# Kernel tuning notes

Hardware: AMD Instinct MI355X
Metric: run time of the kernel (lower is better)

## Reference

```python
import jax, jax.numpy as jnp
import numpy as np

B, H, S, D = 2, 16, 2048, 64
EMBED_SIZE = 64
NEG_INF = -1e9


def setup_inputs() -> dict:
    key = jax.random.key(0)
    kq, kk, kv, kb = jax.random.split(key, 4)
    Q = jax.random.normal(kq, (B, H, S, D), dtype=jnp.float32)
    K = jax.random.normal(kk, (B, H, S, D), dtype=jnp.float32)
    V = jax.random.normal(kv, (B, H, S, D), dtype=jnp.float32)
    attn_bias = jax.random.normal(kb, (B, H, S, S), dtype=jnp.float32)
    # causal mask: True means masked (matches torch masked_fill semantics)
    causal = ~jnp.tril(jnp.ones((S, S), dtype=bool))
    attn_mask = jnp.broadcast_to(causal, (B, H, S, S))
    return {"Q": Q, "K": K, "V": V, "attn_mask": attn_mask, "attn_bias": attn_bias}


def reference(Q, K, V, attn_mask, attn_bias):
    scale = 1.0 / np.sqrt(EMBED_SIZE).astype(np.float32)
    scores = jnp.einsum("bhqd,bhkd->bhqk", Q, K) * scale  # [B,H,S,S]
    scores = scores + attn_bias
    scores = jnp.where(attn_mask, NEG_INF, scores)
    attn = jax.nn.softmax(scores, axis=-1)
    context = jnp.einsum("bhqk,bhkd->bhqd", attn, V)
    return (context, attn)
```

## Files before the change

kernel.cpp:

```cpp
#include <hip/hip_runtime.h>


typedef __attribute__((ext_vector_type(4))) float  f32x4;
typedef __attribute__((ext_vector_type(8))) short  short8;
typedef __attribute__((ext_vector_type(4))) short  short4v;

#define S_DIM 2048
#define D_DIM 64
#define QB    16

__device__ __forceinline__ unsigned short f2bf(float f) {
  unsigned u = __builtin_bit_cast(unsigned, f);
  u = (u + 0x7FFFu + ((u >> 16) & 1u)) >> 16;
  return (unsigned short)u;
}
__device__ __forceinline__ float bf2f(unsigned short s) {
  unsigned u = ((unsigned)s) << 16;
  return __builtin_bit_cast(float, u);
}

__launch_bounds__(256, 2)
__global__ void sdpa_kernel(const float* __restrict__ Qg,
                            const float* __restrict__ Kg,
                            const float* __restrict__ Vg,
                            const float* __restrict__ Bg,
                            float* __restrict__ ctx_out,
                            float* __restrict__ attn_out) {
  __shared__ unsigned short plds[QB * S_DIM];
  __shared__ unsigned short vt[D_DIM * 72];
  __shared__ float rowsum[QB];

  const int tid  = threadIdx.x;
  const int lane = tid & 63;
  const int wave = tid >> 6;
  const int l15  = lane & 15;
  const int l4   = lane >> 4;

  const int qtile = 127 - (int)blockIdx.x;
  const int bh    = blockIdx.y;
  const int qbase = qtile * QB;

  if (tid < QB) rowsum[tid] = 0.0f;
  __syncthreads();

  const float* qrow = Qg + ((size_t)bh * S_DIM + (size_t)(qbase + l15)) * D_DIM;
  short8 qfrag[2];
#pragma unroll
  for (int t = 0; t < 2; ++t) {
    const f32x4* p = (const f32x4*)(qrow + t * 32 + l4 * 8);
    f32x4 a = p[0], b = p[1];
    short8 f;
#pragma unroll
    for (int j = 0; j < 4; ++j) {
      f[j]     = (short)f2bf(a[j] * 0.125f);
      f[j + 4] = (short)f2bf(b[j] * 0.125f);
    }
    qfrag[t] = f;
  }

  const int nkt = ((qbase + QB - 1) >> 6) + 1;
  const float* Kbh = Kg + (size_t)bh * S_DIM * D_DIM;
  const float* Bbh = Bg + (size_t)bh * S_DIM * S_DIM;

  float rsv[4] = {0.f, 0.f, 0.f, 0.f};

  for (int kt = 0; kt < nkt; ++kt) {
    const int kg = kt * 64 + wave * 16 + l15;
    const float* krow = Kbh + (size_t)kg * D_DIM;
    short8 kfrag[2];
#pragma unroll
    for (int t = 0; t < 2; ++t) {
      const f32x4* p = (const f32x4*)(krow + t * 32 + l4 * 8);
      f32x4 a = p[0], b = p[1];
      short8 f;
#pragma unroll
      for (int j = 0; j < 4; ++j) {
        f[j]     = (short)f2bf(a[j]);
        f[j + 4] = (short)f2bf(b[j]);
      }
      kfrag[t] = f;
    }
    float bv[4];
#pragma unroll
    for (int r = 0; r < 4; ++r) {
      const int q = qbase + l4 * 4 + r;
      bv[r] = Bbh[(size_t)q * S_DIM + kg];
    }
    f32x4 acc = {0.f, 0.f, 0.f, 0.f};
    acc = __builtin_amdgcn_mfma_f32_16x16x32_bf16(qfrag[0], kfrag[0], acc, 0, 0, 0);
    acc = __builtin_amdgcn_mfma_f32_16x16x32_bf16(qfrag[1], kfrag[1], acc, 0, 0, 0);
#pragma unroll
    for (int r = 0; r < 4; ++r) {
      const int qi = l4 * 4 + r;
      const int q  = qbase + qi;
      const float pval = (kg <= q) ? __expf(acc[r] + bv[r]) : 0.0f;
      rsv[r] += pval;
      const int idx = (qi * S_DIM + kg) ^ ((qi & 7) << 3);
      plds[idx] = f2bf(pval);
    }
  }

#pragma unroll
  for (int r = 0; r < 4; ++r) {
    float v = rsv[r];
    v += __shfl_xor(v, 1);
    v += __shfl_xor(v, 2);
    v += __shfl_xor(v, 4);
    v += __shfl_xor(v, 8);
    if (l15 == 0) atomicAdd(&rowsum[l4 * 4 + r], v);
  }
  __syncthreads();

  float* abase = attn_out + ((size_t)bh * S_DIM + (size_t)qbase) * S_DIM;
  for (int qi = 0; qi < QB; ++qi) {
    const int qg = qbase + qi;
    const float inv = __builtin_amdgcn_rcpf(rowsum[qi]);
    float* arow = abase + (size_t)qi * S_DIM;
#pragma unroll
    for (int half = 0; half < 2; ++half) {
      const int kc = (half * 256 + tid) * 4;
      f32x4 o;
      if (kc > qg) {
        o = (f32x4){0.f, 0.f, 0.f, 0.f};
      } else {
        const int idx = (qi * S_DIM + kc) ^ ((qi & 7) << 3);
        short4v sv = *(const short4v*)&plds[idx];
#pragma unroll
        for (int j = 0; j < 4; ++j)
          o[j] = (kc + j <= qg) ? bf2f((unsigned short)sv[j]) * inv : 0.f;
      }
      *(f32x4*)(arow + kc) = o;
    }
  }

  f32x4 cacc = {0.f, 0.f, 0.f, 0.f};
  const float* Vbh = Vg + (size_t)bh * S_DIM * D_DIM;
  const int dbase = wave * 16;
  for (int kt = 0; kt < nkt; ++kt) {
    const float* vrow = Vbh + ((size_t)(kt * 64 + lane)) * D_DIM + dbase;
    f32x4 v0 = ((const f32x4*)vrow)[0];
    f32x4 v1 = ((const f32x4*)vrow)[1];
    f32x4 v2 = ((const f32x4*)vrow)[2];
    f32x4 v3 = ((const f32x4*)vrow)[3];
#pragma unroll
    for (int j = 0; j < 4; ++j) {
      vt[(dbase + j)      * 72 + lane] = f2bf(v0[j]);
      vt[(dbase + 4 + j)  * 72 + lane] = f2bf(v1[j]);
      vt[(dbase + 8 + j)  * 72 + lane] = f2bf(v2[j]);
      vt[(dbase + 12 + j) * 72 + lane] = f2bf(v3[j]);
    }
#pragma unroll
    for (int t = 0; t < 2; ++t) {
      const int kk   = kt * 64 + t * 32 + l4 * 8;
      const int aidx = (l15 * S_DIM + kk) ^ ((l15 & 7) << 3);
      short8 af = *(const short8*)&plds[aidx];
      short8 bf = *(const short8*)&vt[(dbase + l15) * 72 + t * 32 + l4 * 8];
      cacc = __builtin_amdgcn_mfma_f32_16x16x32_bf16(af, bf, cacc, 0, 0, 0);
    }
  }

  float* cbase = ctx_out + ((size_t)bh * S_DIM + (size_t)qbase) * D_DIM + dbase + l15;
#pragma unroll
  for (int r = 0; r < 4; ++r) {
    const int qi = l4 * 4 + r;
    const float inv = __builtin_amdgcn_rcpf(rowsum[qi]);
    cbase[(size_t)qi * D_DIM] = cacc[r] * inv;
  }
}

extern "C" void kernel_launch(void* const* d_in, const int* in_sizes, int n_in,
                              void* d_out, int out_size, void* d_ws, size_t ws_size,
                              hipStream_t stream) {
  (void)in_sizes; (void)n_in; (void)out_size; (void)d_ws; (void)ws_size;
  const float* Q    = (const float*)d_in[0];
  const float* K    = (const float*)d_in[1];
  const float* V    = (const float*)d_in[2];
  const float* bias = (const float*)d_in[4];

  float* ctx  = (float*)d_out;
  float* attn = (float*)d_out + (size_t)2 * 16 * 2048 * 64;

  dim3 grid(128, 32);
  dim3 block(256);
  sdpa_kernel<<<grid, block, 0, stream>>>(Q, K, V, bias, ctx, attn);
}
```

Before: 1.276 ms.

## Keep probabilities in registers, shrink LDS, use 512-thread blocks for occupancy

Replaces the full 16x2048 bf16 probability buffer in LDS with packed per-thread register storage and a small per-key-tile staging tile. This cuts LDS use so more blocks fit per CU. Blocks grow to 512 threads, with 128-wide key tiles and the PV product split across two wave halves that are reduced through LDS. The masked upper region of attn is zero-filled up front with nontemporal stores, and bias loads and attn writes also become nontemporal. In exchange it adds two barriers per key tile, reads V directly from global with strided scalar loads, and raises register pressure from the unrolled packed-P array.

```diff
diff --git a/kernel.cpp b/kernel.cpp
--- a/kernel.cpp
+++ b/kernel.cpp
@@ -3,11 +3,13 @@
 
 typedef __attribute__((ext_vector_type(4))) float  f32x4;
 typedef __attribute__((ext_vector_type(8))) short  short8;
-typedef __attribute__((ext_vector_type(4))) short  short4v;
-
-#define S_DIM 2048
-#define D_DIM 64
-#define QB    16
+
+#define S_DIM   2048
+#define QB      16
+#define KTW     128
+#define MAXNKT  16
+#define PSTR    136
+#define CSTR    68
 
 __device__ __forceinline__ unsigned short f2bf(float f) {
   unsigned u = __builtin_bit_cast(unsigned, f);
@@ -19,15 +21,15 @@
   return __builtin_bit_cast(float, u);
 }
 
-__launch_bounds__(256, 2)
+__launch_bounds__(512, 4)
 __global__ void sdpa_kernel(const float* __restrict__ Qg,
                             const float* __restrict__ Kg,
                             const float* __restrict__ Vg,
                             const float* __restrict__ Bg,
                             float* __restrict__ ctx_out,
                             float* __restrict__ attn_out) {
-  __shared__ unsigned short plds[QB * S_DIM];
-  __shared__ unsigned short vt[D_DIM * 72];
+  __shared__ alignas(16) unsigned short ptile[QB * PSTR];
+  __shared__ float ctile[QB * CSTR];
   __shared__ float rowsum[QB];
 
   const int tid  = threadIdx.x;
@@ -39,11 +41,23 @@
   const int qtile = 127 - (int)blockIdx.x;
   const int bh    = blockIdx.y;
   const int qbase = qtile * QB;
+  const int nkt   = ((qbase + QB - 1) >> 7) + 1;
 
   if (tid < QB) rowsum[tid] = 0.0f;
+
+  float* abase = attn_out + ((size_t)bh * S_DIM + (size_t)qbase) * S_DIM;
+  {
+    const int c = nkt * KTW + (tid << 2);
+    if (c < S_DIM) {
+      const f32x4 z = {0.f, 0.f, 0.f, 0.f};
+#pragma unroll
+      for (int qi = 0; qi < QB; ++qi)
+        __builtin_nontemporal_store(z, (f32x4*)(abase + (size_t)qi * S_DIM + c));
+    }
+  }
   __syncthreads();
 
-  const float* qrow = Qg + ((size_t)bh * S_DIM + (size_t)(qbase + l15)) * D_DIM;
+  const float* qrow = Qg + ((size_t)bh * S_DIM + (size_t)(qbase + l15)) * 64;
   short8 qfrag[2];
 #pragma unroll
   for (int t = 0; t < 2; ++t) {
@@ -58,45 +72,47 @@
     qfrag[t] = f;
   }
 
-  const int nkt = ((qbase + QB - 1) >> 6) + 1;
-  const float* Kbh = Kg + (size_t)bh * S_DIM * D_DIM;
+  const float* Kbh = Kg + (size_t)bh * S_DIM * 64;
   const float* Bbh = Bg + (size_t)bh * S_DIM * S_DIM;
 
   float rsv[4] = {0.f, 0.f, 0.f, 0.f};
-
-  for (int kt = 0; kt < nkt; ++kt) {
-    const int kg = kt * 64 + wave * 16 + l15;
-    const float* krow = Kbh + (size_t)kg * D_DIM;
-    short8 kfrag[2];
-#pragma unroll
-    for (int t = 0; t < 2; ++t) {
-      const f32x4* p = (const f32x4*)(krow + t * 32 + l4 * 8);
-      f32x4 a = p[0], b = p[1];
-      short8 f;
-#pragma unroll
-      for (int j = 0; j < 4; ++j) {
-        f[j]     = (short)f2bf(a[j]);
-        f[j + 4] = (short)f2bf(b[j]);
-      }
-      kfrag[t] = f;
-    }
-    float bv[4];
-#pragma unroll
-    for (int r = 0; r < 4; ++r) {
-      const int q = qbase + l4 * 4 + r;
-      bv[r] = Bbh[(size_t)q * S_DIM + kg];
-    }
-    f32x4 acc = {0.f, 0.f, 0.f, 0.f};
-    acc = __builtin_amdgcn_mfma_f32_16x16x32_bf16(qfrag[0], kfrag[0], acc, 0, 0, 0);
-    acc = __builtin_amdgcn_mfma_f32_16x16x32_bf16(qfrag[1], kfrag[1], acc, 0, 0, 0);
-#pragma unroll
-    for (int r = 0; r < 4; ++r) {
-      const int qi = l4 * 4 + r;
-      const int q  = qbase + qi;
-      const float pval = (kg <= q) ? __expf(acc[r] + bv[r]) : 0.0f;
-      rsv[r] += pval;
-      const int idx = (qi * S_DIM + kg) ^ ((qi & 7) << 3);
-      plds[idx] = f2bf(pval);
+  unsigned p_pk[MAXNKT][2];
+
+#pragma unroll
+  for (int kt = 0; kt < MAXNKT; ++kt) {
+    if (kt < nkt) {
+      const int kg = kt * KTW + (wave << 4) + l15;
+      const float* krow = Kbh + (size_t)kg * 64;
+      short8 kfrag[2];
+#pragma unroll
+      for (int t = 0; t < 2; ++t) {
+        const f32x4* p = (const f32x4*)(krow + t * 32 + l4 * 8);
+        f32x4 a = p[0], b = p[1];
+        short8 f;
+#pragma unroll
+        for (int j = 0; j < 4; ++j) {
+          f[j]     = (short)f2bf(a[j]);
+          f[j + 4] = (short)f2bf(b[j]);
+        }
+        kfrag[t] = f;
+      }
+      float bv[4];
+#pragma unroll
+      for (int r = 0; r < 4; ++r)
+        bv[r] = __builtin_nontemporal_load(
+                  &Bbh[(size_t)(qbase + l4 * 4 + r) * S_DIM + kg]);
+      f32x4 acc = {0.f, 0.f, 0.f, 0.f};
+      acc = __builtin_amdgcn_mfma_f32_16x16x32_bf16(qfrag[0], kfrag[0], acc, 0, 0, 0);
+      acc = __builtin_amdgcn_mfma_f32_16x16x32_bf16(qfrag[1], kfrag[1], acc, 0, 0, 0);
+      float pv[4];
+#pragma unroll
+      for (int r = 0; r < 4; ++r) {
+        const int q = qbase + l4 * 4 + r;
+        pv[r] = (kg <= q) ? __expf(acc[r] + bv[r]) : 0.0f;
+        rsv[r] += pv[r];
+      }
+      p_pk[kt][0] = (unsigned)f2bf(pv[0]) | ((unsigned)f2bf(pv[1]) << 16);
+      p_pk[kt][1] = (unsigned)f2bf(pv[2]) | ((unsigned)f2bf(pv[3]) << 16);
     }
   }
 
@@ -111,60 +127,62 @@
   }
   __syncthreads();
 
-  float* abase = attn_out + ((size_t)bh * S_DIM + (size_t)qbase) * S_DIM;
-  for (int qi = 0; qi < QB; ++qi) {
-    const int qg = qbase + qi;
-    const float inv = __builtin_amdgcn_rcpf(rowsum[qi]);
-    float* arow = abase + (size_t)qi * S_DIM;
-#pragma unroll
-    for (int half = 0; half < 2; ++half) {
-      const int kc = (half * 256 + tid) * 4;
-      f32x4 o;
-      if (kc > qg) {
-        o = (f32x4){0.f, 0.f, 0.f, 0.f};
-      } else {
-        const int idx = (qi * S_DIM + kc) ^ ((qi & 7) << 3);
-        short4v sv = *(const short4v*)&plds[idx];
-#pragma unroll
-        for (int j = 0; j < 4; ++j)
-          o[j] = (kc + j <= qg) ? bf2f((unsigned short)sv[j]) * inv : 0.f;
-      }
-      *(f32x4*)(arow + kc) = o;
-    }
-  }
+  float invv[4];
+#pragma unroll
+  for (int r = 0; r < 4; ++r)
+    invv[r] = __builtin_amdgcn_rcpf(rowsum[l4 * 4 + r]);
 
   f32x4 cacc = {0.f, 0.f, 0.f, 0.f};
-  const float* Vbh = Vg + (size_t)bh * S_DIM * D_DIM;
-  const int dbase = wave * 16;
-  for (int kt = 0; kt < nkt; ++kt) {
-    const float* vrow = Vbh + ((size_t)(kt * 64 + lane)) * D_DIM + dbase;
-    f32x4 v0 = ((const f32x4*)vrow)[0];
-    f32x4 v1 = ((const f32x4*)vrow)[1];
-    f32x4 v2 = ((const f32x4*)vrow)[2];
-    f32x4 v3 = ((const f32x4*)vrow)[3];
-#pragma unroll
-    for (int j = 0; j < 4; ++j) {
-      vt[(dbase + j)      * 72 + lane] = f2bf(v0[j]);
-      vt[(dbase + 4 + j)  * 72 + lane] = f2bf(v1[j]);
-      vt[(dbase + 8 + j)  * 72 + lane] = f2bf(v2[j]);
-      vt[(dbase + 12 + j) * 72 + lane] = f2bf(v3[j]);
-    }
-#pragma unroll
-    for (int t = 0; t < 2; ++t) {
-      const int kk   = kt * 64 + t * 32 + l4 * 8;
-      const int aidx = (l15 * S_DIM + kk) ^ ((l15 & 7) << 3);
-      short8 af = *(const short8*)&plds[aidx];
-      short8 bf = *(const short8*)&vt[(dbase + l15) * 72 + t * 32 + l4 * 8];
-      cacc = __builtin_amdgcn_mfma_f32_16x16x32_bf16(af, bf, cacc, 0, 0, 0);
-    }
-  }
-
-  float* cbase = ctx_out + ((size_t)bh * S_DIM + (size_t)qbase) * D_DIM + dbase + l15;
-#pragma unroll
-  for (int r = 0; r < 4; ++r) {
-    const int qi = l4 * 4 + r;
-    const float inv = __builtin_amdgcn_rcpf(rowsum[qi]);
-    cbase[(size_t)qi * D_DIM] = cacc[r] * inv;
+  const float* Vbh = Vg + (size_t)bh * S_DIM * 64;
+  const int d0    = (wave & 3) << 4;
+  const int chalf = (wave >> 2) << 1;
+  const int wcol  = (wave << 4) + l15;
+
+#pragma unroll
+  for (int kt = 0; kt < MAXNKT; ++kt) {
+    if (kt < nkt) {
+#pragma unroll
+      for (int r = 0; r < 4; ++r) {
+        const int qi = l4 * 4 + r;
+        const unsigned pk = p_pk[kt][r >> 1];
+        const unsigned short pb =
+            (r & 1) ? (unsigned short)(pk >> 16) : (unsigned short)(pk & 0xFFFFu);
+        ptile[qi * PSTR + wcol] = pb;
+        __builtin_nontemporal_store(
+            bf2f(pb) * invv[r],
+            abase + (size_t)qi * S_DIM + (size_t)(kt * KTW + wcol));
+      }
+      __syncthreads();
+#pragma unroll
+      for (int ci = 0; ci < 2; ++ci) {
+        const int c = chalf + ci;
+        short8 af = *(const short8*)&ptile[l15 * PSTR + c * 32 + l4 * 8];
+        const float* vbase =
+            Vbh + (size_t)(kt * KTW + c * 32 + l4 * 8) * 64 + d0 + l15;
+        short8 bfv;
+#pragma unroll
+        for (int j = 0; j < 8; ++j)
+          bfv[j] = (short)f2bf(vbase[(size_t)j * 64]);
+        cacc = __builtin_amdgcn_mfma_f32_16x16x32_bf16(af, bfv, cacc, 0, 0, 0);
+      }
+      __syncthreads();
+    }
+  }
+
+  if (wave < 4) {
+#pragma unroll
+    for (int r = 0; r < 4; ++r)
+      ctile[(l4 * 4 + r) * CSTR + d0 + l15] = cacc[r];
+  }
+  __syncthreads();
+  if (wave >= 4) {
+    float* cbase = ctx_out + ((size_t)bh * S_DIM + (size_t)qbase) * 64;
+#pragma unroll
+    for (int r = 0; r < 4; ++r) {
+      const int qi = l4 * 4 + r;
+      cbase[(size_t)qi * 64 + d0 + l15] =
+          (ctile[qi * CSTR + d0 + l15] + cacc[r]) * invv[r];
+    }
   }
 }
 
@@ -181,6 +199,6 @@
   float* attn = (float*)d_out + (size_t)2 * 16 * 2048 * 64;
 
   dim3 grid(128, 32);
-  dim3 block(256);
+  dim3 block(512);
   sdpa_kernel<<<grid, block, 0, stream>>>(Q, K, V, bias, ctx, attn);
 }
```

New measurement: 1.244 ms. 1.03x faster.
